# Kernel tuning notes

Hardware: AMD Instinct MI355X
Metric: run time of the kernel (lower is better)

Reference implementation:

```python
import jax, jax.numpy as jnp
import numpy as np
from jax import lax

UNITS = [100, 80, 50, 30]
IN_FEAT = 64

def setup_inputs() -> dict:
    key = jax.random.key(0)
    ks = jax.random.split(key, 16)
    B, T, F = 512, 512, IN_FEAT
    ins = [F] + UNITS[:-1]
    d = {"x": jax.random.normal(ks[0], (B, T, F), jnp.float32)}
    for li, (u, fi) in enumerate(zip(UNITS, ins)):
        din = u + fi  # concat([h, x]) per the cell
        scale = 1.0 / np.sqrt(din)
        d[f"W{li}"] = jax.random.normal(ks[1 + li], (din, 4 * u), jnp.float32) * scale
        d[f"b{li}"] = jnp.zeros((4 * u,), jnp.float32)
    d["Wout"] = jax.random.normal(ks[10], (UNITS[-1], 1), jnp.float32) * (1.0 / np.sqrt(UNITS[-1]))
    d["bout"] = jnp.zeros((1,), jnp.float32)
    return d

def _lstm_layer(x, W, b, units, return_sequences):
    # x: [B, T, F] -> hidden sequence [B, T, units] or last hidden [B, units]
    B = x.shape[0]
    h0 = jnp.zeros((B, units), x.dtype)
    c0 = jnp.zeros((B, units), x.dtype)

    def step(carry, xt):
        h, c = carry
        z = jnp.concatenate([h, xt], axis=-1) @ W + b  # [B, 4u]
        f, i, g, o = jnp.split(z, 4, axis=-1)  # gate order: forget, input, candidate, output
        f = jax.nn.sigmoid(f)
        i = jax.nn.sigmoid(i)
        g = jnp.tanh(g)
        c_new = f * c + i * g
        h_new = jax.nn.sigmoid(o) * jnp.tanh(c_new)
        return (h_new, c_new), (h_new if return_sequences else None)

    xs = jnp.swapaxes(x, 0, 1)  # [T, B, F]
    (h_last, _), hs = lax.scan(step, (h0, c0), xs)
    if return_sequences:
        return jnp.swapaxes(hs, 0, 1)  # [B, T, units]
    return h_last

def reference(x, W0, b0, W1, b1, W2, b2, W3, b3, Wout, bout):
    # Dropout layers are identity at inference (training=False).
    h = _lstm_layer(x, W0, b0, UNITS[0], True)
    h = _lstm_layer(h, W1, b1, UNITS[1], True)
    h = _lstm_layer(h, W2, b2, UNITS[2], True)
    h = _lstm_layer(h, W3, b3, UNITS[3], False)  # last-layer RNN returns final hidden only
    return h @ Wout + bout  # [B, 1]
```

## Files before the change

### kernel.cpp

```cpp
#include <hip/hip_runtime.h>


#define T_SEQ 512
#define B_TOT 512

__device__ __forceinline__ float sigmoidf_(float x) {
    return 1.0f / (1.0f + __expf(-x));
}
__device__ __forceinline__ float tanh_fast(float x) {
    float e = __expf(2.0f * x);
    return 1.0f - 2.0f / (1.0f + e);
}

template<int U, int FI, int S, int KH, int BLOCK, bool SEQ, bool FINAL>
__global__ __launch_bounds__(BLOCK, 2)
void lstm_layer(const float* __restrict__ X,
                const float* __restrict__ W,
                const float* __restrict__ Bv,
                float* __restrict__ Hout,
                const float* __restrict__ Wd,
                const float* __restrict__ bd,
                float* __restrict__ OUT)
{
    constexpr int DIN  = U + FI;
    constexpr int DIN4 = S * KH;
    static_assert(DIN4 >= DIN, "k-padding must cover DIN");
    static_assert((KH & 1) == 0, "KH even: one float4 = 2 k x 2 rows");
    constexpr int G  = 4 * U;
    constexpr int NT = S * U;
    static_assert(NT <= BLOCK, "GEMV threads must fit");
    static_assert(NT >= 2 * FI, "prefetch threads must be GEMV threads");
    constexpr int TOT = 2 * DIN4;

    __shared__ __align__(16) float buf[2][TOT];
    __shared__ __align__(16) float zp[S * 2 * U * 4];

    const int tid = threadIdx.x;
    const int bb  = blockIdx.x * 2;

    const int p = tid % U;
    const int s = tid / U;

    float w[4][KH];
    if (tid < NT) {
        #pragma unroll
        for (int g = 0; g < 4; ++g) {
            #pragma unroll
            for (int kk = 0; kk < KH; ++kk) {
                const int k = s * KH + kk;
                w[g][kk] = (k < DIN) ? W[(size_t)k * G + g * U + p] : 0.0f;
            }
        }
    }

    float cb4[4] = {0.f, 0.f, 0.f, 0.f};
    if (tid < 2 * U) {
        #pragma unroll
        for (int g = 0; g < 4; ++g) cb4[g] = Bv[g * U + p];
    }
    float hreg = 0.0f, creg = 0.0f;
    float wdreg = 0.0f;
    if constexpr (FINAL) { if (tid < 2 * U) wdreg = Wd[p]; }

    const int xr = (tid < FI) ? 0 : 1;
    const int xj = tid - xr * FI;
    const float* Xrow = X + (size_t)(bb + xr) * T_SEQ * FI + xj;
    const int xwi = 2 * (U + xj) + xr;

    for (int i = tid; i < 2 * TOT; i += BLOCK) ((float*)buf)[i] = 0.0f;
    __syncthreads();
    if (tid < 2 * FI) buf[0][xwi] = Xrow[0];
    __syncthreads();

    const int rbase = s * (KH / 2);

    for (int t = 0; t < T_SEQ; ++t) {
        const int cur = t & 1, nxt = cur ^ 1;

        float xpre = 0.0f;
        const bool do_x = (tid < 2 * FI) && (t + 1 < T_SEQ);
        if (do_x) xpre = Xrow[(size_t)(t + 1) * FI];

        if (tid < NT) {
            float a0 = 0.f, a1 = 0.f, a2 = 0.f, a3 = 0.f;
            float b0 = 0.f, b1 = 0.f, b2 = 0.f, b3 = 0.f;
            const float4* rb = (const float4*)buf[cur];
            #pragma unroll
            for (int q = 0; q < KH / 2; ++q) {
                const float4 v = rb[rbase + q];
                a0 += w[0][2*q] * v.x; b0 += w[0][2*q] * v.y;
                a1 += w[1][2*q] * v.x; b1 += w[1][2*q] * v.y;
                a2 += w[2][2*q] * v.x; b2 += w[2][2*q] * v.y;
                a3 += w[3][2*q] * v.x; b3 += w[3][2*q] * v.y;
                a0 += w[0][2*q+1] * v.z; b0 += w[0][2*q+1] * v.w;
                a1 += w[1][2*q+1] * v.z; b1 += w[1][2*q+1] * v.w;
                a2 += w[2][2*q+1] * v.z; b2 += w[2][2*q+1] * v.w;
                a3 += w[3][2*q+1] * v.z; b3 += w[3][2*q+1] * v.w;
            }
            float4* zq = (float4*)zp;
            zq[(s * 2 + 0) * U + p] = make_float4(a0, a1, a2, a3);
            zq[(s * 2 + 1) * U + p] = make_float4(b0, b1, b2, b3);
        }
        if (do_x) buf[nxt][xwi] = xpre;
        __syncthreads();

        if (tid < 2 * U) {
            float z0 = cb4[0], z1 = cb4[1], z2 = cb4[2], z3 = cb4[3];
            const float4* zq = (const float4*)zp;
            #pragma unroll
            for (int ss = 0; ss < S; ++ss) {
                const float4 v = zq[(ss * 2 + s) * U + p];
                z0 += v.x; z1 += v.y; z2 += v.z; z3 += v.w;
            }
            const float F  = sigmoidf_(z0);
            const float I  = sigmoidf_(z1);
            const float Gv = tanh_fast(z2);
            const float O  = sigmoidf_(z3);
            creg = F * creg + I * Gv;
            hreg = O * tanh_fast(creg);
            buf[nxt][2 * p + s] = hreg;
            if constexpr (SEQ) {
                Hout[((size_t)(bb + s) * T_SEQ + t) * U + p] = hreg;
            }
        }
        __syncthreads();
    }

    if constexpr (FINAL) {
        if (tid < 2 * U) buf[0][2 * p + s] = hreg * wdreg;
        __syncthreads();
        if (tid < 2) {
            float acc = bd[0];
            for (int u = 0; u < U; ++u) acc += buf[0][2 * u + tid];
            OUT[bb + tid] = acc;
        }
    }
}

extern "C" void kernel_launch(void* const* d_in, const int* in_sizes, int n_in,
                              void* d_out, int out_size, void* d_ws, size_t ws_size,
                              hipStream_t stream)
{
    const float* x    = (const float*)d_in[0];
    const float* W0   = (const float*)d_in[1];
    const float* b0   = (const float*)d_in[2];
    const float* W1   = (const float*)d_in[3];
    const float* b1   = (const float*)d_in[4];
    const float* W2   = (const float*)d_in[5];
    const float* b2   = (const float*)d_in[6];
    const float* W3   = (const float*)d_in[7];
    const float* b3   = (const float*)d_in[8];
    const float* Wout = (const float*)d_in[9];
    const float* bout = (const float*)d_in[10];
    float* out = (float*)d_out;

    float* H0 = (float*)d_ws;
    float* H1 = H0 + (size_t)B_TOT * T_SEQ * 100;
    float* H2 = (float*)d_ws;

    const dim3 grid(B_TOT / 2);

    hipLaunchKernelGGL((lstm_layer<100,  64, 5, 36, 512, true,  false>),
                       grid, dim3(512), 0, stream, x,  W0, b0, H0, nullptr, nullptr, nullptr);
    hipLaunchKernelGGL((lstm_layer< 80, 100, 6, 30, 512, true,  false>),
                       grid, dim3(512), 0, stream, H0, W1, b1, H1, nullptr, nullptr, nullptr);
    hipLaunchKernelGGL((lstm_layer< 50,  80, 5, 26, 256, true,  false>),
                       grid, dim3(256), 0, stream, H1, W2, b2, H2, nullptr, nullptr, nullptr);
    hipLaunchKernelGGL((lstm_layer< 30,  50, 8, 10, 256, false, true >),
                       grid, dim3(256), 0, stream, H2, W3, b3, nullptr, Wout, bout, out);
}
```

Baseline: 1.955 ms.

## Move half of LSTM gate weights to LDS and widen K-split for small layers

```diff
diff --git a/kernel.cpp b/kernel.cpp
--- a/kernel.cpp
+++ b/kernel.cpp
@@ -12,7 +12,7 @@
     return 1.0f - 2.0f / (1.0f + e);
 }
 
-template<int U, int FI, int S, int KH, int BLOCK, bool SEQ, bool FINAL>
+template<int U, int FI, int S, int KH, int BLOCK, int LG, bool SEQ, bool FINAL>
 __global__ __launch_bounds__(BLOCK, 2)
 void lstm_layer(const float* __restrict__ X,
                 const float* __restrict__ W,
@@ -28,12 +28,16 @@
     static_assert((KH & 1) == 0, "KH even: one float4 = 2 k x 2 rows");
     constexpr int G  = 4 * U;
     constexpr int NT = S * U;
+    constexpr int Q  = KH / 2;
+    constexpr int RG = 4 - LG;
     static_assert(NT <= BLOCK, "GEMV threads must fit");
     static_assert(NT >= 2 * FI, "prefetch threads must be GEMV threads");
+    static_assert(LG == 0 || LG == 2, "LG in {0,2}");
     constexpr int TOT = 2 * DIN4;
 
-    __shared__ __align__(16) float buf[2][TOT];
-    __shared__ __align__(16) float zp[S * 2 * U * 4];
+    __shared__ __align__(16) float  buf[2][TOT];
+    __shared__ __align__(16) float  zp[S * 2 * U * 4];
+    __shared__ __align__(16) float4 wl[LG ? Q * NT : 1];
 
     const int tid = threadIdx.x;
     const int bb  = blockIdx.x * 2;
@@ -41,14 +45,29 @@
     const int p = tid % U;
     const int s = tid / U;
 
-    float w[4][KH];
+    float w[RG][KH];
     if (tid < NT) {
         #pragma unroll
-        for (int g = 0; g < 4; ++g) {
+        for (int g = 0; g < RG; ++g) {
             #pragma unroll
             for (int kk = 0; kk < KH; ++kk) {
                 const int k = s * KH + kk;
-                w[g][kk] = (k < DIN) ? W[(size_t)k * G + g * U + p] : 0.0f;
+                w[g][kk] = (k < DIN) ? W[(size_t)k * G + (LG + g) * U + p] : 0.0f;
+            }
+        }
+    }
+
+    if constexpr (LG == 2) {
+        if (tid < NT) {
+            #pragma unroll
+            for (int q = 0; q < Q; ++q) {
+                const int k0 = s * KH + 2 * q, k1 = k0 + 1;
+                float4 wv;
+                wv.x = (k0 < DIN) ? W[(size_t)k0 * G + 0 * U + p] : 0.0f;
+                wv.y = (k1 < DIN) ? W[(size_t)k1 * G + 0 * U + p] : 0.0f;
+                wv.z = (k0 < DIN) ? W[(size_t)k0 * G + 1 * U + p] : 0.0f;
+                wv.w = (k1 < DIN) ? W[(size_t)k1 * G + 1 * U + p] : 0.0f;
+                wl[q * NT + tid] = wv;
             }
         }
     }
@@ -72,7 +91,7 @@
     if (tid < 2 * FI) buf[0][xwi] = Xrow[0];
     __syncthreads();
 
-    const int rbase = s * (KH / 2);
+    const int rbase = s * Q;
 
     for (int t = 0; t < T_SEQ; ++t) {
         const int cur = t & 1, nxt = cur ^ 1;
@@ -86,16 +105,28 @@
             float b0 = 0.f, b1 = 0.f, b2 = 0.f, b3 = 0.f;
             const float4* rb = (const float4*)buf[cur];
             #pragma unroll
-            for (int q = 0; q < KH / 2; ++q) {
+            for (int q = 0; q < Q; ++q) {
                 const float4 v = rb[rbase + q];
-                a0 += w[0][2*q] * v.x; b0 += w[0][2*q] * v.y;
-                a1 += w[1][2*q] * v.x; b1 += w[1][2*q] * v.y;
-                a2 += w[2][2*q] * v.x; b2 += w[2][2*q] * v.y;
-                a3 += w[3][2*q] * v.x; b3 += w[3][2*q] * v.y;
-                a0 += w[0][2*q+1] * v.z; b0 += w[0][2*q+1] * v.w;
-                a1 += w[1][2*q+1] * v.z; b1 += w[1][2*q+1] * v.w;
-                a2 += w[2][2*q+1] * v.z; b2 += w[2][2*q+1] * v.w;
-                a3 += w[3][2*q+1] * v.z; b3 += w[3][2*q+1] * v.w;
+                if constexpr (LG == 2) {
+                    const float4 wv = wl[q * NT + tid];
+                    a0 += wv.x * v.x; b0 += wv.x * v.y;
+                    a0 += wv.y * v.z; b0 += wv.y * v.w;
+                    a1 += wv.z * v.x; b1 += wv.z * v.y;
+                    a1 += wv.w * v.z; b1 += wv.w * v.w;
+                    a2 += w[0][2*q]   * v.x; b2 += w[0][2*q]   * v.y;
+                    a2 += w[0][2*q+1] * v.z; b2 += w[0][2*q+1] * v.w;
+                    a3 += w[1][2*q]   * v.x; b3 += w[1][2*q]   * v.y;
+                    a3 += w[1][2*q+1] * v.z; b3 += w[1][2*q+1] * v.w;
+                } else {
+                    a0 += w[0][2*q] * v.x; b0 += w[0][2*q] * v.y;
+                    a1 += w[1][2*q] * v.x; b1 += w[1][2*q] * v.y;
+                    a2 += w[2][2*q] * v.x; b2 += w[2][2*q] * v.y;
+                    a3 += w[3][2*q] * v.x; b3 += w[3][2*q] * v.y;
+                    a0 += w[0][2*q+1] * v.z; b0 += w[0][2*q+1] * v.w;
+                    a1 += w[1][2*q+1] * v.z; b1 += w[1][2*q+1] * v.w;
+                    a2 += w[2][2*q+1] * v.z; b2 += w[2][2*q+1] * v.w;
+                    a3 += w[3][2*q+1] * v.z; b3 += w[3][2*q+1] * v.w;
+                }
             }
             float4* zq = (float4*)zp;
             zq[(s * 2 + 0) * U + p] = make_float4(a0, a1, a2, a3);
@@ -160,12 +191,12 @@
 
     const dim3 grid(B_TOT / 2);
 
-    hipLaunchKernelGGL((lstm_layer<100,  64, 5, 36, 512, true,  false>),
+    hipLaunchKernelGGL((lstm_layer<100,  64,  5, 34, 512, 2, true,  false>),
                        grid, dim3(512), 0, stream, x,  W0, b0, H0, nullptr, nullptr, nullptr);
-    hipLaunchKernelGGL((lstm_layer< 80, 100, 6, 30, 512, true,  false>),
+    hipLaunchKernelGGL((lstm_layer< 80, 100,  6, 30, 512, 2, true,  false>),
                        grid, dim3(512), 0, stream, H0, W1, b1, H1, nullptr, nullptr, nullptr);
-    hipLaunchKernelGGL((lstm_layer< 50,  80, 5, 26, 256, true,  false>),
-                       grid, dim3(256), 0, stream, H1, W2, b2, H2, nullptr, nullptr, nullptr);
-    hipLaunchKernelGGL((lstm_layer< 30,  50, 8, 10, 256, false, true >),
-                       grid, dim3(256), 0, stream, H2, W3, b3, nullptr, Wout, bout, out);
-}
+    hipLaunchKernelGGL((lstm_layer< 50,  80, 10, 14, 512, 0, true,  false>),
+                       grid, dim3(512), 0, stream, H1, W2, b2, H2, nullptr, nullptr, nullptr);
+    hipLaunchKernelGGL((lstm_layer< 30,  50, 16,  6, 512, 0, false, true >),
+                       grid, dim3(512), 0, stream, H2, W3, b3, nullptr, Wout, bout, out);
+}
```

Measured after the change: 2.305 ms. 1.18x slower.
